# Kernel optimization log

Measured on AMD Instinct MI355X. Metric: run time of the kernel, lower is better.

## Reference

```python
import jax, jax.numpy as jnp
import numpy as np

N_NODES = 100000
N_EDGES = 1600000
NODE_DIM = 24
EDGE_DIM = 2
HIDDEN = 128


def _glorot(key, shape):
    fan_in, fan_out = shape[0], shape[1]
    lim = (6.0 / (fan_in + fan_out)) ** 0.5
    return jax.random.uniform(key, shape, jnp.float32, -lim, lim)


def setup_inputs() -> dict:
    key = jax.random.key(0)
    ks = jax.random.split(key, 8)
    x = jax.random.normal(ks[0], (N_NODES, NODE_DIM), jnp.float32)
    edge_index = jax.random.randint(ks[1], (2, N_EDGES), 0, N_NODES, jnp.int64)
    edge_attr = jax.random.normal(ks[2], (N_EDGES, EDGE_DIM), jnp.float32)
    # params
    W_in = _glorot(ks[3], (NODE_DIM, HIDDEN)); b_in = jnp.zeros((HIDDEN,), jnp.float32)
    W_e = _glorot(ks[4], (EDGE_DIM, HIDDEN)); b_e = jnp.zeros((HIDDEN,), jnp.float32)
    # nn_update is SHARED between conv1 and conv2 in the torch module
    W1 = _glorot(ks[5], (HIDDEN, HIDDEN)); b1 = jnp.zeros((HIDDEN,), jnp.float32)
    W2 = _glorot(ks[6], (HIDDEN, HIDDEN)); b2 = jnp.zeros((HIDDEN,), jnp.float32)
    return {"x": x, "edge_index": edge_index, "edge_attr": edge_attr,
            "W_in": W_in, "b_in": b_in, "W_e": W_e, "b_e": b_e,
            "W1": W1, "b1": b1, "W2": W2, "b2": b2}


def _gine_conv(h, src, dst, e, W1, b1, W2, b2):
    # message: relu(h_j + e_ij), aggregate: sum at dst; eps = 0 (GINEConv default)
    msg = jax.nn.relu(h[src] + e)                      # [E, H]
    agg = jax.ops.segment_sum(msg, dst, num_segments=N_NODES)  # [N, H]
    z = h + agg                                        # (1+eps)*h + agg, eps=0
    return jnp.maximum(z @ W1 + b1, 0.0) @ W2 + b2


def reference(x, edge_index, edge_attr, W_in, b_in, W_e, b_e, W1, b1, W2, b2):
    src, dst = edge_index[0], edge_index[1]
    h = x @ W_in + b_in                    # [N, H]
    e = edge_attr @ W_e + b_e              # [E, H]
    h = _gine_conv(h, src, dst, e, W1, b1, W2, b2)
    h = jax.nn.relu(h)
    h = _gine_conv(h, src, dst, e, W1, b1, W2, b2)
    return h
```

## Files before the change

kernel.cpp:

```cpp
#include <hip/hip_runtime.h>

#define N_NODES 100000
#define N_EDGES 1600000
#define NODE_DIM 24
#define HIDDEN 128
#define BSHIFT 9
#define NBUCK 196
#define BCAP 10240
#define P1_EDGES 2048
#define TILE 32
#define LREC 1024
#define NI_BLOCKS 2048

typedef __attribute__((ext_vector_type(8))) short bf16x8;
typedef __attribute__((ext_vector_type(4))) float f32x4;

__device__ __forceinline__ ushort f2bf(float f) {
  uint u = __builtin_bit_cast(uint, f);
  u += 0x7fffu + ((u >> 16) & 1u);
  return (ushort)(u >> 16);
}
__device__ __forceinline__ float bflo(uint v) { return __builtin_bit_cast(float, v << 16); }
__device__ __forceinline__ float bfhi(uint v) { return __builtin_bit_cast(float, v & 0xffff0000u); }

__global__ __launch_bounds__(256) void prep_kernel(
    const float* __restrict__ x, const float* __restrict__ W_in,
    const float* __restrict__ b_in, const float* __restrict__ W1,
    const float* __restrict__ W2, uint* __restrict__ hb32,
    ushort* __restrict__ W1t, ushort* __restrict__ W2t) {
  if (blockIdx.x >= NI_BLOCKS) {
    const int i = (blockIdx.x - NI_BLOCKS) * 256 + threadIdx.x;
    if (i < HIDDEN * HIDDEN) {
      const int k = i >> 7, n = i & 127;
      W1t[n * HIDDEN + k] = f2bf(W1[k * HIDDEN + n]);
      W2t[n * HIDDEN + k] = f2bf(W2[k * HIDDEN + n]);
    }
    return;
  }
  __shared__ float w_lds[NODE_DIM * HIDDEN];
  __shared__ float b_lds[HIDDEN];
  for (int i = threadIdx.x; i < NODE_DIM * HIDDEN; i += 256) w_lds[i] = W_in[i];
  if (threadIdx.x < HIDDEN) b_lds[threadIdx.x] = b_in[threadIdx.x];
  __syncthreads();
  const int l = threadIdx.x & 63;
  const int g = threadIdx.x >> 6;
  const int j0 = l * 2;
  for (int n = blockIdx.x * 4 + g; n < N_NODES; n += NI_BLOCKS * 4) {
    float a0 = b_lds[j0], a1 = b_lds[j0 + 1];
    const float* xr = x + (size_t)n * NODE_DIM;
#pragma unroll
    for (int d = 0; d < NODE_DIM; ++d) {
      const float xv = xr[d];
      a0 = fmaf(xv, w_lds[d * HIDDEN + j0], a0);
      a1 = fmaf(xv, w_lds[d * HIDDEN + j0 + 1], a1);
    }
    hb32[(size_t)n * 64 + l] = (uint)f2bf(a0) | ((uint)f2bf(a1) << 16);
  }
}

__global__ __launch_bounds__(256) void k_bucket_scatter(
    const int* __restrict__ srcs, const int* __restrict__ dsts,
    const float2* __restrict__ ea2, int* __restrict__ gcur,
    uint2* __restrict__ tmp) {
  __shared__ int hist[256];
  __shared__ int sc[256];
  __shared__ int lofs[256];
  __shared__ int base[256];
  __shared__ int cur2[256];
  __shared__ uint2 stage[P1_EDGES];
  __shared__ uchar stage_b[P1_EDGES];
  const int t = threadIdx.x;
  const int e0 = blockIdx.x * P1_EDGES;

  hist[t] = 0;
  cur2[t] = 0;
  __syncthreads();

  uint rw0[8], rw1[8];
  int rb[8];
#pragma unroll
  for (int i = 0; i < 8; ++i) {
    const int e = e0 + t + i * 256;
    if (e < N_EDGES) {
      const int s = srcs[e];
      const int d = dsts[e];
      const float2 a = ea2[e];
      const int b = d >> BSHIFT;
      rb[i] = b;
      rw0[i] = (uint)s | ((uint)(d & 511) << 20);
      rw1[i] = (uint)f2bf(a.x) | ((uint)f2bf(a.y) << 16);
      atomicAdd(&hist[b], 1);
    } else {
      rb[i] = -1;
    }
  }
  __syncthreads();

  int v = hist[t];
  sc[t] = v;
  __syncthreads();
  for (int d = 1; d < 256; d <<= 1) {
    int x = (t >= d) ? sc[t - d] : 0;
    __syncthreads();
    sc[t] += x;
    __syncthreads();
  }
  lofs[t] = sc[t] - v;
  base[t] = (t < NBUCK && v > 0) ? atomicAdd(&gcur[t], v) : 0;
  __syncthreads();

#pragma unroll
  for (int i = 0; i < 8; ++i) {
    if (rb[i] >= 0) {
      const int l = atomicAdd(&cur2[rb[i]], 1);
      const int slot = lofs[rb[i]] + l;
      stage[slot] = make_uint2(rw0[i], rw1[i]);
      stage_b[slot] = (uchar)rb[i];
    }
  }
  __syncthreads();

  const int total = (N_EDGES - e0 < P1_EDGES) ? (N_EDGES - e0) : P1_EDGES;
  for (int s = t; s < total; s += 256) {
    const int b = stage_b[s];
    const int idx = base[b] + (s - lofs[b]);
    if (idx < BCAP) tmp[(size_t)b * BCAP + idx] = stage[s];
  }
}

__global__ __launch_bounds__(256) void k_bucket_base(
    const int* __restrict__ gcur, int* __restrict__ gbase,
    int* __restrict__ off) {
  __shared__ int s[256];
  const int t = threadIdx.x;
  int v = (t < NBUCK) ? gcur[t] : 0;
  s[t] = v;
  __syncthreads();
  for (int d = 1; d < 256; d <<= 1) {
    int x = (t >= d) ? s[t - d] : 0;
    __syncthreads();
    s[t] += x;
    __syncthreads();
  }
  if (t < NBUCK) gbase[t] = s[t] - v;
  if (t == 0) off[N_NODES] = N_EDGES;
}

__global__ __launch_bounds__(256) void k_bucket_sort(
    const uint2* __restrict__ tmp, const int* __restrict__ gcur,
    const int* __restrict__ gbase, int* __restrict__ off,
    uint2* __restrict__ rec) {
  __shared__ int lcnt[512];
  __shared__ int lofs[512];
  __shared__ int lcur[512];
  __shared__ int psc[256];
  const int t = threadIdx.x;
  const int b = blockIdx.x;
  const int nb0 = b << BSHIFT;
  const uint2* __restrict__ btmp = tmp + (size_t)b * BCAP;
  int cnt = gcur[b];
  if (cnt > BCAP) cnt = BCAP;
  const int base = gbase[b];

  lcnt[t] = 0;
  lcnt[t + 256] = 0;
  __syncthreads();
  for (int s = t; s < cnt; s += 256) {
    atomicAdd(&lcnt[(btmp[s].x >> 20) & 511], 1);
  }
  __syncthreads();
  const int a0 = lcnt[2 * t], a1 = lcnt[2 * t + 1];
  const int p = a0 + a1;
  psc[t] = p;
  __syncthreads();
  for (int d = 1; d < 256; d <<= 1) {
    int x = (t >= d) ? psc[t - d] : 0;
    __syncthreads();
    psc[t] += x;
    __syncthreads();
  }
  const int ep = psc[t] - p;
  lofs[2 * t] = ep;
  lofs[2 * t + 1] = ep + a0;
  lcur[2 * t] = ep;
  lcur[2 * t + 1] = ep + a0;
  __syncthreads();
  for (int i = t; i < 512; i += 256) {
    const int n = nb0 + i;
    if (n < N_NODES) off[n] = base + lofs[i];
  }
  for (int s = t; s < cnt; s += 256) {
    const uint2 r = btmp[s];
    const int dl = (r.x >> 20) & 511;
    const int pp = atomicAdd(&lcur[dl], 1);
    rec[base + pp] = make_uint2(r.x & 0xFFFFFu, r.y);
  }
}

__global__ __launch_bounds__(256) void conv_fused(
    const int* __restrict__ off, const uint2* __restrict__ rec,
    const float* __restrict__ W_e, const float* __restrict__ b_e,
    const uint4* __restrict__ hb4, const ushort* __restrict__ W1t,
    const ushort* __restrict__ W2t, const float* __restrict__ bias1,
    const float* __restrict__ bias2, float* __restrict__ outf,
    ushort* __restrict__ outb, const int relu_out) {
  __shared__ short zs[TILE][136];
  __shared__ uint2 lrec[LREC];
  __shared__ int loff[TILE + 1];
  const int tid = threadIdx.x;
  const int lane = tid & 63;
  const int wave = tid >> 6;
  const int l15 = lane & 15;
  const int grp = lane >> 4;
  const int n0 = blockIdx.x * TILE;

  if (tid <= TILE) loff[tid] = off[n0 + tid];
  const int rbase = off[n0];
  const int rend = off[n0 + TILE];
  const int rcnt = rend - rbase;
  const bool staged = (rcnt <= LREC);
  if (staged) {
    for (int i = tid; i < rcnt; i += 256) lrec[i] = rec[rbase + i];
  }

  const int j0 = l15 * 8;
  float we0[8], we1[8], beq[8];
#pragma unroll
  for (int k = 0; k < 8; ++k) {
    we0[k] = W_e[j0 + k];
    we1[k] = W_e[HIDDEN + j0 + k];
    beq[k] = b_e[j0 + k];
  }
  __syncthreads();

  {
    auto gather = [&](auto readrec) {
      for (int i = 0; i < 8; ++i) {
        const int n = n0 + wave * 8 + i;
        float acc[8];
#pragma unroll
        for (int k = 0; k < 8; ++k) acc[k] = 0.f;
        const int o = loff[wave * 8 + i] - rbase;
        const int dn = loff[wave * 8 + i + 1] - loff[wave * 8 + i];
        const int nfull = dn >> 2;

        int c = 0;
        for (; c + 2 <= nfull; c += 2) {
          const uint2 r0 = readrec(o + c * 4 + grp);
          const uint2 r1 = readrec(o + c * 4 + 4 + grp);
          const uint4 hv0 = hb4[(size_t)r0.x * 16 + l15];
          const uint4 hv1 = hb4[(size_t)r1.x * 16 + l15];
          {
            const float ex = bflo(r0.y), ey = bfhi(r0.y);
            const uint hw[4] = {hv0.x, hv0.y, hv0.z, hv0.w};
#pragma unroll
            for (int k = 0; k < 4; ++k) {
              const float c0 = fmaf(ex, we0[2 * k], fmaf(ey, we1[2 * k], beq[2 * k]));
              const float c1 = fmaf(ex, we0[2 * k + 1], fmaf(ey, we1[2 * k + 1], beq[2 * k + 1]));
              acc[2 * k] += fmaxf(bflo(hw[k]) + c0, 0.f);
              acc[2 * k + 1] += fmaxf(bfhi(hw[k]) + c1, 0.f);
            }
          }
          {
            const float ex = bflo(r1.y), ey = bfhi(r1.y);
            const uint hw[4] = {hv1.x, hv1.y, hv1.z, hv1.w};
#pragma unroll
            for (int k = 0; k < 4; ++k) {
              const float c0 = fmaf(ex, we0[2 * k], fmaf(ey, we1[2 * k], beq[2 * k]));
              const float c1 = fmaf(ex, we0[2 * k + 1], fmaf(ey, we1[2 * k + 1], beq[2 * k + 1]));
              acc[2 * k] += fmaxf(bflo(hw[k]) + c0, 0.f);
              acc[2 * k + 1] += fmaxf(bfhi(hw[k]) + c1, 0.f);
            }
          }
        }
        if (c < nfull) {
          const uint2 r0 = readrec(o + c * 4 + grp);
          const uint4 hv0 = hb4[(size_t)r0.x * 16 + l15];
          const float ex = bflo(r0.y), ey = bfhi(r0.y);
          const uint hw[4] = {hv0.x, hv0.y, hv0.z, hv0.w};
#pragma unroll
          for (int k = 0; k < 4; ++k) {
            const float c0 = fmaf(ex, we0[2 * k], fmaf(ey, we1[2 * k], beq[2 * k]));
            const float c1 = fmaf(ex, we0[2 * k + 1], fmaf(ey, we1[2 * k + 1], beq[2 * k + 1]));
            acc[2 * k] += fmaxf(bflo(hw[k]) + c0, 0.f);
            acc[2 * k + 1] += fmaxf(bfhi(hw[k]) + c1, 0.f);
          }
        }
        const int ntail = dn & 3;
        if (grp < ntail) {
          const uint2 r0 = readrec(o + nfull * 4 + grp);
          const uint4 hv0 = hb4[(size_t)r0.x * 16 + l15];
          const float ex = bflo(r0.y), ey = bfhi(r0.y);
          const uint hw[4] = {hv0.x, hv0.y, hv0.z, hv0.w};
#pragma unroll
          for (int k = 0; k < 4; ++k) {
            const float c0 = fmaf(ex, we0[2 * k], fmaf(ey, we1[2 * k], beq[2 * k]));
            const float c1 = fmaf(ex, we0[2 * k + 1], fmaf(ey, we1[2 * k + 1], beq[2 * k + 1]));
            acc[2 * k] += fmaxf(bflo(hw[k]) + c0, 0.f);
            acc[2 * k + 1] += fmaxf(bfhi(hw[k]) + c1, 0.f);
          }
        }

#pragma unroll
        for (int k = 0; k < 8; ++k) {
          float v = acc[k];
          v += __shfl_xor(v, 16, 64);
          v += __shfl_xor(v, 32, 64);
          acc[k] = v;
        }
        const uint4 hs = hb4[(size_t)n * 16 + l15];
        acc[0] += bflo(hs.x); acc[1] += bfhi(hs.x);
        acc[2] += bflo(hs.y); acc[3] += bfhi(hs.y);
        acc[4] += bflo(hs.z); acc[5] += bfhi(hs.z);
        acc[6] += bflo(hs.w); acc[7] += bfhi(hs.w);

        uint p0, p1, p2, p3;
        asm("v_cvt_pk_bf16_f32 %0, %1, %2" : "=v"(p0) : "v"(acc[0]), "v"(acc[1]));
        asm("v_cvt_pk_bf16_f32 %0, %1, %2" : "=v"(p1) : "v"(acc[2]), "v"(acc[3]));
        asm("v_cvt_pk_bf16_f32 %0, %1, %2" : "=v"(p2) : "v"(acc[4]), "v"(acc[5]));
        asm("v_cvt_pk_bf16_f32 %0, %1, %2" : "=v"(p3) : "v"(acc[6]), "v"(acc[7]));
        if (grp == 0) {
          *(uint4*)&zs[wave * 8 + i][l15 * 8] = make_uint4(p0, p1, p2, p3);
        }
      }
    };
    if (staged) {
      gather([&](int i) -> uint2 { return lrec[i]; });
    } else {
      gather([&](int i) -> uint2 { return rec[rbase + i]; });
    }
  }
  __syncthreads();

  const int kq = grp;
  const int colbase = wave * 32;
  const int c0 = colbase + l15, c1 = colbase + 16 + l15;

  f32x4 acc[2][2];
  {
    const float bb0 = bias1[c0], bb1 = bias1[c1];
#pragma unroll
    for (int mt = 0; mt < 2; ++mt) {
      acc[mt][0] = (f32x4){bb0, bb0, bb0, bb0};
      acc[mt][1] = (f32x4){bb1, bb1, bb1, bb1};
    }
  }
#pragma unroll
  for (int kt = 0; kt < 4; ++kt) {
    const int kk = kt * 32 + kq * 8;
    const bf16x8 bf0 = *(const bf16x8*)&W1t[(size_t)c0 * HIDDEN + kk];
    const bf16x8 bf1 = *(const bf16x8*)&W1t[(size_t)c1 * HIDDEN + kk];
#pragma unroll
    for (int mt = 0; mt < 2; ++mt) {
      const bf16x8 a = *(const bf16x8*)&zs[mt * 16 + l15][kk];
      acc[mt][0] = __builtin_amdgcn_mfma_f32_16x16x32_bf16(a, bf0, acc[mt][0], 0, 0, 0);
      acc[mt][1] = __builtin_amdgcn_mfma_f32_16x16x32_bf16(a, bf1, acc[mt][1], 0, 0, 0);
    }
  }
  __syncthreads();
#pragma unroll
  for (int mt = 0; mt < 2; ++mt)
#pragma unroll
    for (int nt = 0; nt < 2; ++nt)
#pragma unroll
      for (int r = 0; r < 4; ++r) {
        const int row = mt * 16 + kq * 4 + r;
        const int col = colbase + nt * 16 + l15;
        float v = acc[mt][nt][r];
        zs[row][col] = (short)f2bf(v > 0.f ? v : 0.f);
      }
  __syncthreads();

  {
    const float bb0 = bias2[c0], bb1 = bias2[c1];
#pragma unroll
    for (int mt = 0; mt < 2; ++mt) {
      acc[mt][0] = (f32x4){bb0, bb0, bb0, bb0};
      acc[mt][1] = (f32x4){bb1, bb1, bb1, bb1};
    }
  }
#pragma unroll
  for (int kt = 0; kt < 4; ++kt) {
    const int kk = kt * 32 + kq * 8;
    const bf16x8 bf0 = *(const bf16x8*)&W2t[(size_t)c0 * HIDDEN + kk];
    const bf16x8 bf1 = *(const bf16x8*)&W2t[(size_t)c1 * HIDDEN + kk];
#pragma unroll
    for (int mt = 0; mt < 2; ++mt) {
      const bf16x8 a = *(const bf16x8*)&zs[mt * 16 + l15][kk];
      acc[mt][0] = __builtin_amdgcn_mfma_f32_16x16x32_bf16(a, bf0, acc[mt][0], 0, 0, 0);
      acc[mt][1] = __builtin_amdgcn_mfma_f32_16x16x32_bf16(a, bf1, acc[mt][1], 0, 0, 0);
    }
  }
#pragma unroll
  for (int mt = 0; mt < 2; ++mt)
#pragma unroll
    for (int nt = 0; nt < 2; ++nt)
#pragma unroll
      for (int r = 0; r < 4; ++r) {
        const int row = mt * 16 + kq * 4 + r;
        const int col = colbase + nt * 16 + l15;
        float v = acc[mt][nt][r];
        if (relu_out) v = v > 0.f ? v : 0.f;
        if (outf) outf[(size_t)(n0 + row) * HIDDEN + col] = v;
        if (outb) outb[(size_t)(n0 + row) * HIDDEN + col] = f2bf(v);
      }
}

__global__ __launch_bounds__(256) void node_init_f32(
    const float* __restrict__ x, const float* __restrict__ W_in,
    const float* __restrict__ b_in, float* __restrict__ h) {
  __shared__ float w_lds[NODE_DIM * HIDDEN];
  __shared__ float b_lds[HIDDEN];
  for (int i = threadIdx.x; i < NODE_DIM * HIDDEN; i += 256) w_lds[i] = W_in[i];
  if (threadIdx.x < HIDDEN) b_lds[threadIdx.x] = b_in[threadIdx.x];
  __syncthreads();
  const int j = threadIdx.x & 127;
  const int g = threadIdx.x >> 7;
  for (int n = blockIdx.x * 2 + g; n < N_NODES; n += gridDim.x * 2) {
    float acc = b_lds[j];
    const float* xr = x + (size_t)n * NODE_DIM;
#pragma unroll
    for (int d = 0; d < NODE_DIM; ++d) acc = fmaf(xr[d], w_lds[d * HIDDEN + j], acc);
    h[(size_t)n * HIDDEN + j] = acc;
  }
}

__global__ __launch_bounds__(256) void edge_scatter_kernel(
    const int* __restrict__ ei, const float* __restrict__ ea,
    const float* __restrict__ W_e, const float* __restrict__ b_e,
    const float* __restrict__ h, float* __restrict__ agg) {
  const int j = threadIdx.x & 127;
  const int g = threadIdx.x >> 7;
  const float we0 = W_e[j];
  const float we1 = W_e[HIDDEN + j];
  const float be = b_e[j];
  const int* __restrict__ srcs = ei;
  const int* __restrict__ dsts = ei + N_EDGES;
  const float2* __restrict__ ea2 = (const float2*)ea;
  for (int e = blockIdx.x * 2 + g; e < N_EDGES; e += gridDim.x * 2) {
    const int s = srcs[e];
    const int d = dsts[e];
    const float2 a = ea2[e];
    float m = h[(size_t)s * HIDDEN + j] + fmaf(a.x, we0, fmaf(a.y, we1, be));
    m = m > 0.f ? m : 0.f;
    unsafeAtomicAdd(&agg[(size_t)d * HIDDEN + j], m);
  }
}

template <bool RELU_OUT>
__global__ __launch_bounds__(256) void mlp_f32_kernel(
    const float* __restrict__ zbuf, const float* __restrict__ agg,
    const float* __restrict__ W1, const float* __restrict__ b1,
    const float* __restrict__ W2, const float* __restrict__ b2,
    float* __restrict__ out) {
  const int NB = 32;
  const int NT = 16;
  __shared__ float zs[NB][HIDDEN];
  __shared__ float ts[NB][HIDDEN];
  const int j = threadIdx.x & 127;
  const int g = threadIdx.x >> 7;
  const int n0 = blockIdx.x * NB;

#pragma unroll
  for (int n = 0; n < NT; ++n) {
    const int nn = g * NT + n;
    zs[nn][j] = zbuf[(size_t)(n0 + nn) * HIDDEN + j] + agg[(size_t)(n0 + nn) * HIDDEN + j];
  }
  __syncthreads();

  float acc[NT];
  const float b1j = b1[j];
#pragma unroll
  for (int n = 0; n < NT; ++n) acc[n] = b1j;
  for (int k = 0; k < HIDDEN; k += 4) {
    const float w0 = W1[(k + 0) * HIDDEN + j];
    const float w1 = W1[(k + 1) * HIDDEN + j];
    const float w2 = W1[(k + 2) * HIDDEN + j];
    const float w3 = W1[(k + 3) * HIDDEN + j];
#pragma unroll
    for (int n = 0; n < NT; ++n) {
      const float4 z = *reinterpret_cast<const float4*>(&zs[g * NT + n][k]);
      acc[n] = fmaf(z.x, w0, acc[n]);
      acc[n] = fmaf(z.y, w1, acc[n]);
      acc[n] = fmaf(z.z, w2, acc[n]);
      acc[n] = fmaf(z.w, w3, acc[n]);
    }
  }
#pragma unroll
  for (int n = 0; n < NT; ++n) ts[g * NT + n][j] = acc[n] > 0.f ? acc[n] : 0.f;
  __syncthreads();

  const float b2j = b2[j];
#pragma unroll
  for (int n = 0; n < NT; ++n) acc[n] = b2j;
  for (int k = 0; k < HIDDEN; k += 4) {
    const float w0 = W2[(k + 0) * HIDDEN + j];
    const float w1 = W2[(k + 1) * HIDDEN + j];
    const float w2 = W2[(k + 2) * HIDDEN + j];
    const float w3 = W2[(k + 3) * HIDDEN + j];
#pragma unroll
    for (int n = 0; n < NT; ++n) {
      const float4 z = *reinterpret_cast<const float4*>(&ts[g * NT + n][k]);
      acc[n] = fmaf(z.x, w0, acc[n]);
      acc[n] = fmaf(z.y, w1, acc[n]);
      acc[n] = fmaf(z.z, w2, acc[n]);
      acc[n] = fmaf(z.w, w3, acc[n]);
    }
  }
#pragma unroll
  for (int n = 0; n < NT; ++n) {
    float v = acc[n];
    if (RELU_OUT) v = v > 0.f ? v : 0.f;
    out[(size_t)(n0 + g * NT + n) * HIDDEN + j] = v;
  }
}

extern "C" void kernel_launch(void* const* d_in, const int* in_sizes, int n_in,
                              void* d_out, int out_size, void* d_ws, size_t ws_size,
                              hipStream_t stream) {
  const float* x    = (const float*)d_in[0];
  const int*   ei   = (const int*)d_in[1];
  const float* ea   = (const float*)d_in[2];
  const float* W_in = (const float*)d_in[3];
  const float* b_in = (const float*)d_in[4];
  const float* W_e  = (const float*)d_in[5];
  const float* b_e  = (const float*)d_in[6];
  const float* W1   = (const float*)d_in[7];
  const float* b1   = (const float*)d_in[8];
  const float* W2   = (const float*)d_in[9];
  const float* b2   = (const float*)d_in[10];

  const int* srcs = ei;
  const int* dsts = ei + N_EDGES;
  const float2* ea2 = (const float2*)ea;

  float* h = (float*)d_out;
  char* ws = (char*)d_ws;

  const size_t OFF_OFF  = 0;
  const size_t GCUR_OFF = 402432;
  const size_t GBAS_OFF = 406528;
  const size_t WT1_OFF  = 410624;
  const size_t WT2_OFF  = 443392;
  const size_t REC_OFF  = 1048576;
  const size_t HBA_OFF  = REC_OFF + 12800000;
  const size_t TMP_OFF  = HBA_OFF + 25600000;
  const size_t HBB_OFF  = TMP_OFF;
  const size_t need = HBB_OFF + 25600000;

  if (ws_size >= need) {
    int* off     = (int*)(ws + OFF_OFF);
    int* gcur    = (int*)(ws + GCUR_OFF);
    int* gbase   = (int*)(ws + GBAS_OFF);
    ushort* W1t  = (ushort*)(ws + WT1_OFF);
    ushort* W2t  = (ushort*)(ws + WT2_OFF);
    uint2* rec   = (uint2*)(ws + REC_OFF);
    ushort* hba  = (ushort*)(ws + HBA_OFF);
    uint2* tmp   = (uint2*)(ws + TMP_OFF);
    ushort* hbb  = (ushort*)(ws + HBB_OFF);

    prep_kernel<<<NI_BLOCKS + 64, 256, 0, stream>>>(x, W_in, b_in, W1, W2,
                                                    (uint*)hba, W1t, W2t);
    hipMemsetAsync(gcur, 0, NBUCK * sizeof(int), stream);
    k_bucket_scatter<<<(N_EDGES + P1_EDGES - 1) / P1_EDGES, 256, 0, stream>>>(
        srcs, dsts, ea2, gcur, tmp);
    k_bucket_base<<<1, 256, 0, stream>>>(gcur, gbase, off);
    k_bucket_sort<<<NBUCK, 256, 0, stream>>>(tmp, gcur, gbase, off, rec);

    const int cblocks = N_NODES / TILE;
    conv_fused<<<cblocks, 256, 0, stream>>>(off, rec, W_e, b_e,
                                            (const uint4*)hba, W1t, W2t, b1, b2,
                                            nullptr, hbb, 1);
    conv_fused<<<cblocks, 256, 0, stream>>>(off, rec, W_e, b_e,
                                            (const uint4*)hbb, W1t, W2t, b1, b2,
                                            h, nullptr, 0);
  } else {
    float* agg = (float*)d_ws;
    const size_t agg_bytes = (size_t)N_NODES * HIDDEN * sizeof(float);

    node_init_f32<<<2048, 256, 0, stream>>>(x, W_in, b_in, h);

    hipMemsetAsync(agg, 0, agg_bytes, stream);
    edge_scatter_kernel<<<4096, 256, 0, stream>>>(ei, ea, W_e, b_e, h, agg);
    mlp_f32_kernel<true><<<N_NODES / 32, 256, 0, stream>>>(h, agg, W1, b1, W2, b2, h);

    hipMemsetAsync(agg, 0, agg_bytes, stream);
    edge_scatter_kernel<<<4096, 256, 0, stream>>>(ei, ea, W_e, b_e, h, agg);
    mlp_f32_kernel<false><<<N_NODES / 32, 256, 0, stream>>>(h, agg, W1, b1, W2, b2, h);
  }
}
```

Measured before the change: 278.7 us.

## Fold bucket memset and base scan into neighbors, deepen gather load batching

Zeroing the bucket counters moves into an extra block of prep_kernel, replacing the separate memset. The single-block prefix-scan kernel is removed: each bucket_sort block recomputes the 196-entry scan in shared memory. The edge gather loop now issues loads for up to four edge chunks at once before doing the math, to raise memory-level parallelism. Together these remove two launches and add more in-flight loads per wave, at the cost of redundant scans and possibly higher register pressure.

Result: slower. 291.5 us (+4.6%).

```diff
diff --git a/kernel.cpp b/kernel.cpp
--- a/kernel.cpp
+++ b/kernel.cpp
@@ -15,6 +15,8 @@
 typedef __attribute__((ext_vector_type(8))) short bf16x8;
 typedef __attribute__((ext_vector_type(4))) float f32x4;
 
+template <int N> struct IC { static constexpr int value = N; };
+
 __device__ __forceinline__ ushort f2bf(float f) {
   uint u = __builtin_bit_cast(uint, f);
   u += 0x7fffu + ((u >> 16) & 1u);
@@ -27,9 +29,15 @@
     const float* __restrict__ x, const float* __restrict__ W_in,
     const float* __restrict__ b_in, const float* __restrict__ W1,
     const float* __restrict__ W2, uint* __restrict__ hb32,
-    ushort* __restrict__ W1t, ushort* __restrict__ W2t) {
+    ushort* __restrict__ W1t, ushort* __restrict__ W2t,
+    int* __restrict__ gcur) {
   if (blockIdx.x >= NI_BLOCKS) {
-    const int i = (blockIdx.x - NI_BLOCKS) * 256 + threadIdx.x;
+    const int bx = blockIdx.x - NI_BLOCKS;
+    if (bx >= 64) {
+      if (threadIdx.x < NBUCK) gcur[threadIdx.x] = 0;
+      return;
+    }
+    const int i = bx * 256 + threadIdx.x;
     if (i < HIDDEN * HIDDEN) {
       const int k = i >> 7, n = i & 127;
       W1t[n * HIDDEN + k] = f2bf(W1[k * HIDDEN + n]);
@@ -128,28 +136,10 @@
   }
 }
 
-__global__ __launch_bounds__(256) void k_bucket_base(
-    const int* __restrict__ gcur, int* __restrict__ gbase,
-    int* __restrict__ off) {
-  __shared__ int s[256];
-  const int t = threadIdx.x;
-  int v = (t < NBUCK) ? gcur[t] : 0;
-  s[t] = v;
-  __syncthreads();
-  for (int d = 1; d < 256; d <<= 1) {
-    int x = (t >= d) ? s[t - d] : 0;
-    __syncthreads();
-    s[t] += x;
-    __syncthreads();
-  }
-  if (t < NBUCK) gbase[t] = s[t] - v;
-  if (t == 0) off[N_NODES] = N_EDGES;
-}
-
 __global__ __launch_bounds__(256) void k_bucket_sort(
     const uint2* __restrict__ tmp, const int* __restrict__ gcur,
-    const int* __restrict__ gbase, int* __restrict__ off,
-    uint2* __restrict__ rec) {
+    int* __restrict__ off, uint2* __restrict__ rec) {
+  __shared__ int gsc[256];
   __shared__ int lcnt[512];
   __shared__ int lofs[512];
   __shared__ int lcur[512];
@@ -158,13 +148,24 @@
   const int b = blockIdx.x;
   const int nb0 = b << BSHIFT;
   const uint2* __restrict__ btmp = tmp + (size_t)b * BCAP;
-  int cnt = gcur[b];
-  if (cnt > BCAP) cnt = BCAP;
-  const int base = gbase[b];
-
+
+  const int gv = (t < NBUCK) ? gcur[t] : 0;
+  gsc[t] = gv;
   lcnt[t] = 0;
   lcnt[t + 256] = 0;
   __syncthreads();
+  for (int d = 1; d < 256; d <<= 1) {
+    int x = (t >= d) ? gsc[t - d] : 0;
+    __syncthreads();
+    gsc[t] += x;
+    __syncthreads();
+  }
+  const int rawcnt = gcur[b];
+  const int base = gsc[b] - rawcnt;
+  int cnt = rawcnt;
+  if (cnt > BCAP) cnt = BCAP;
+  if (b == 0 && t == 0) off[N_NODES] = N_EDGES;
+
   for (int s = t; s < cnt; s += 256) {
     atomicAdd(&lcnt[(btmp[s].x >> 20) & 511], 1);
   }
@@ -244,40 +245,9 @@
         const int dn = loff[wave * 8 + i + 1] - loff[wave * 8 + i];
         const int nfull = dn >> 2;
 
-        int c = 0;
-        for (; c + 2 <= nfull; c += 2) {
-          const uint2 r0 = readrec(o + c * 4 + grp);
-          const uint2 r1 = readrec(o + c * 4 + 4 + grp);
-          const uint4 hv0 = hb4[(size_t)r0.x * 16 + l15];
-          const uint4 hv1 = hb4[(size_t)r1.x * 16 + l15];
-          {
-            const float ex = bflo(r0.y), ey = bfhi(r0.y);
-            const uint hw[4] = {hv0.x, hv0.y, hv0.z, hv0.w};
-#pragma unroll
-            for (int k = 0; k < 4; ++k) {
-              const float c0 = fmaf(ex, we0[2 * k], fmaf(ey, we1[2 * k], beq[2 * k]));
-              const float c1 = fmaf(ex, we0[2 * k + 1], fmaf(ey, we1[2 * k + 1], beq[2 * k + 1]));
-              acc[2 * k] += fmaxf(bflo(hw[k]) + c0, 0.f);
-              acc[2 * k + 1] += fmaxf(bfhi(hw[k]) + c1, 0.f);
-            }
-          }
-          {
-            const float ex = bflo(r1.y), ey = bfhi(r1.y);
-            const uint hw[4] = {hv1.x, hv1.y, hv1.z, hv1.w};
-#pragma unroll
-            for (int k = 0; k < 4; ++k) {
-              const float c0 = fmaf(ex, we0[2 * k], fmaf(ey, we1[2 * k], beq[2 * k]));
-              const float c1 = fmaf(ex, we0[2 * k + 1], fmaf(ey, we1[2 * k + 1], beq[2 * k + 1]));
-              acc[2 * k] += fmaxf(bflo(hw[k]) + c0, 0.f);
-              acc[2 * k + 1] += fmaxf(bfhi(hw[k]) + c1, 0.f);
-            }
-          }
-        }
-        if (c < nfull) {
-          const uint2 r0 = readrec(o + c * 4 + grp);
-          const uint4 hv0 = hb4[(size_t)r0.x * 16 + l15];
-          const float ex = bflo(r0.y), ey = bfhi(r0.y);
-          const uint hw[4] = {hv0.x, hv0.y, hv0.z, hv0.w};
+        auto edge_math = [&](uint2 r, uint4 hv) {
+          const float ex = bflo(r.y), ey = bfhi(r.y);
+          const uint hw[4] = {hv.x, hv.y, hv.z, hv.w};
 #pragma unroll
           for (int k = 0; k < 4; ++k) {
             const float c0 = fmaf(ex, we0[2 * k], fmaf(ey, we1[2 * k], beq[2 * k]));
@@ -285,20 +255,28 @@
             acc[2 * k] += fmaxf(bflo(hw[k]) + c0, 0.f);
             acc[2 * k + 1] += fmaxf(bfhi(hw[k]) + c1, 0.f);
           }
-        }
+        };
+        auto do_chunks = [&](int obase, auto cn) {
+          constexpr int C = decltype(cn)::value;
+          uint2 r[C];
+          uint4 hv[C];
+#pragma unroll
+          for (int q = 0; q < C; ++q) r[q] = readrec(obase + q * 4 + grp);
+#pragma unroll
+          for (int q = 0; q < C; ++q) hv[q] = hb4[(size_t)r[q].x * 16 + l15];
+#pragma unroll
+          for (int q = 0; q < C; ++q) edge_math(r[q], hv[q]);
+        };
+
+        int c = 0;
+        for (; c + 4 <= nfull; c += 4) do_chunks(o + c * 4, IC<4>{});
+        if (c + 2 <= nfull) { do_chunks(o + c * 4, IC<2>{}); c += 2; }
+        if (c < nfull) { do_chunks(o + c * 4, IC<1>{}); c += 1; }
         const int ntail = dn & 3;
         if (grp < ntail) {
           const uint2 r0 = readrec(o + nfull * 4 + grp);
           const uint4 hv0 = hb4[(size_t)r0.x * 16 + l15];
-          const float ex = bflo(r0.y), ey = bfhi(r0.y);
-          const uint hw[4] = {hv0.x, hv0.y, hv0.z, hv0.w};
-#pragma unroll
-          for (int k = 0; k < 4; ++k) {
-            const float c0 = fmaf(ex, we0[2 * k], fmaf(ey, we1[2 * k], beq[2 * k]));
-            const float c1 = fmaf(ex, we0[2 * k + 1], fmaf(ey, we1[2 * k + 1], beq[2 * k + 1]));
-            acc[2 * k] += fmaxf(bflo(hw[k]) + c0, 0.f);
-            acc[2 * k + 1] += fmaxf(bfhi(hw[k]) + c1, 0.f);
-          }
+          edge_math(r0, hv0);
         }
 
 #pragma unroll
@@ -539,7 +517,6 @@
 
   const size_t OFF_OFF  = 0;
   const size_t GCUR_OFF = 402432;
-  const size_t GBAS_OFF = 406528;
   const size_t WT1_OFF  = 410624;
   const size_t WT2_OFF  = 443392;
   const size_t REC_OFF  = 1048576;
@@ -551,7 +528,6 @@
   if (ws_size >= need) {
     int* off     = (int*)(ws + OFF_OFF);
     int* gcur    = (int*)(ws + GCUR_OFF);
-    int* gbase   = (int*)(ws + GBAS_OFF);
     ushort* W1t  = (ushort*)(ws + WT1_OFF);
     ushort* W2t  = (ushort*)(ws + WT2_OFF);
     uint2* rec   = (uint2*)(ws + REC_OFF);
@@ -559,13 +535,11 @@
     uint2* tmp   = (uint2*)(ws + TMP_OFF);
     ushort* hbb  = (ushort*)(ws + HBB_OFF);
 
-    prep_kernel<<<NI_BLOCKS + 64, 256, 0, stream>>>(x, W_in, b_in, W1, W2,
-                                                    (uint*)hba, W1t, W2t);
-    hipMemsetAsync(gcur, 0, NBUCK * sizeof(int), stream);
+    prep_kernel<<<NI_BLOCKS + 65, 256, 0, stream>>>(x, W_in, b_in, W1, W2,
+                                                    (uint*)hba, W1t, W2t, gcur);
     k_bucket_scatter<<<(N_EDGES + P1_EDGES - 1) / P1_EDGES, 256, 0, stream>>>(
         srcs, dsts, ea2, gcur, tmp);
-    k_bucket_base<<<1, 256, 0, stream>>>(gcur, gbase, off);
-    k_bucket_sort<<<NBUCK, 256, 0, stream>>>(tmp, gcur, gbase, off, rec);
+    k_bucket_sort<<<NBUCK, 256, 0, stream>>>(tmp, gcur, off, rec);
 
     const int cblocks = N_NODES / TILE;
     conv_fused<<<cblocks, 256, 0, stream>>>(off, rec, W_e, b_e,
```
